# Kernel optimization log

Hardware: AMD Instinct MI355X
Metric: run time of the kernel (lower is better)

## Reference

```python
import jax, jax.numpy as jnp
import numpy as np

N = 100000   # nodes
E = 1600000  # edges (avg degree 16)
F = 128      # num_node_features
H = 128      # hid_size
G = 512      # num graphs in batch
C = 10       # num_classes
D = 32       # graph_degree_distribution.shape[1]
BN_EPS = 1e-5


def setup_inputs() -> dict:
    key = jax.random.key(0)
    ks = jax.random.split(key, 16)
    p = lambda k, shp: jax.random.normal(k, shp, jnp.float32) * 0.02
    x = jax.random.normal(ks[0], (N, F), jnp.float32)
    edge_index = jax.random.randint(ks[1], (2, E), 0, N)
    batch = jnp.sort(jax.random.randint(ks[2], (N,), 0, G))
    degree = jax.random.uniform(ks[3], (N,), jnp.float32) * 10.0
    return dict(
        x=x, edge_index=edge_index, batch=batch, degree=degree,
        eps1=jnp.zeros(()), W1a=p(ks[4], (F, H)), b1a=jnp.zeros(H), W1b=p(ks[5], (H, H)), b1b=jnp.zeros(H),
        g1=jnp.ones(H), be1=jnp.zeros(H),
        eps2=jnp.zeros(()), W2a=p(ks[6], (H, H)), b2a=jnp.zeros(H), W2b=p(ks[7], (H, H)), b2b=jnp.zeros(H),
        g2=jnp.ones(H), be2=jnp.zeros(H),
        Wlin1=p(ks[8], (H, H)), blin1=jnp.zeros(H),
        Wlin2=p(ks[9], (H, C)), blin2=jnp.zeros(C),
        Wlin4=p(ks[10], (H, D)), blin4=jnp.zeros(D),
        Wloss=p(ks[11], (H, 1)), bloss=jnp.zeros(1),
    )


def gin_conv(x, src, dst, eps, Wa, ba, Wb, bb, gamma, beta):
    # GINConv: MLP((1+eps)*x_i + sum_{j->i} x_j); MLP = Lin-ReLU-Lin-ReLU-BN
    agg = jax.ops.segment_sum(x[src], dst, num_segments=x.shape[0])  # [N,F] gather-scatter
    h = (1.0 + eps) * x + agg
    h = jax.nn.relu(h @ Wa + ba)
    h = jax.nn.relu(h @ Wb + bb)
    mu = h.mean(0)
    var = h.var(0)  # biased var, training-mode BN
    return gamma * (h - mu) * jax.lax.rsqrt(var + BN_EPS) + beta


def reference(x, edge_index, batch, degree,
              eps1, W1a, b1a, W1b, b1b, g1, be1,
              eps2, W2a, b2a, W2b, b2b, g2, be2,
              Wlin1, blin1, Wlin2, blin2, Wlin4, blin4, Wloss, bloss):
    src, dst = edge_index[0], edge_index[1]
    h = gin_conv(x, src, dst, eps1, W1a, b1a, W1b, b1b, g1, be1)
    h = gin_conv(h, src, dst, eps2, W2a, b2a, W2b, b2b, g2, be2)
    mse_x = h @ Wloss + bloss                       # [N,1]
    mse_loss = jnp.mean((mse_x - degree[:, None]) ** 2)
    # global_mean_pool over graphs
    sums = jax.ops.segment_sum(h, batch, num_segments=G)
    cnts = jax.ops.segment_sum(jnp.ones((h.shape[0], 1), h.dtype), batch, num_segments=G)
    g = sums / jnp.maximum(cnts, 1.0)               # [G,H]
    z = jax.nn.relu(g @ Wlin1 + blin1)              # dropout inert (eval)
    result1 = jax.nn.log_softmax(z @ Wlin2 + blin2, axis=-1)  # [G,C]
    result3 = z @ Wlin4 + blin4                      # [G,D]
    return result1, result3, mse_loss
```

## Files before the change

kernel.cpp:

```cpp
#include <hip/hip_runtime.h>
#include <hip/hip_bf16.h>

#define HF 128
#define BSH 8
#define BSZ 256
#define NBMAX 1024
#define FCAP 8192
#define AST 136
#define HB 512

typedef __attribute__((ext_vector_type(8))) short bf16x8;
typedef __attribute__((ext_vector_type(4))) float f32x4;
typedef __attribute__((ext_vector_type(2))) float f32x2;

__device__ inline float bflo(unsigned u) { return __uint_as_float(u << 16); }
__device__ inline float bfhi(unsigned u) { return __uint_as_float(u & 0xffff0000u); }
__device__ inline unsigned short f2bf(float f) {
    unsigned u = __float_as_uint(f);
    unsigned r = (u + 0x7fffu + ((u >> 16) & 1u)) >> 16;
    return (unsigned short)r;
}
__device__ inline unsigned pack2(float a, float b) {
    return (unsigned)f2bf(a) | ((unsigned)f2bf(b) << 16);
}
__device__ inline uint2 pk8_fp8(const float* v) {
    int a = __builtin_amdgcn_cvt_pk_fp8_f32(v[0], v[1], 0, 0);
    a = __builtin_amdgcn_cvt_pk_fp8_f32(v[2], v[3], a, 1);
    int b = __builtin_amdgcn_cvt_pk_fp8_f32(v[4], v[5], 0, 0);
    b = __builtin_amdgcn_cvt_pk_fp8_f32(v[6], v[7], b, 1);
    uint2 r; r.x = (unsigned)a; r.y = (unsigned)b;
    return r;
}

__global__ __launch_bounds__(256) void init_all(
    const float* __restrict__ x, unsigned short* __restrict__ xb,
    unsigned char* __restrict__ x8, int castBlk, int nchunks,
    const float* __restrict__ w0, const float* __restrict__ w1,
    const float* __restrict__ w2, const float* __restrict__ w3,
    unsigned short* __restrict__ WtAll,
    const int* __restrict__ dst, int* __restrict__ bpart, int E, int chunkH,
    const int* __restrict__ batch, int* __restrict__ gstart, int N, int Gn, int nBlocks,
    float* __restrict__ Szero, float* __restrict__ outm)
{
    __shared__ int lh[NBMAX];
    int b = blockIdx.x;
    int t = threadIdx.x;
    if (b < castBlk) {
        int i = b * 256 + t;
        if (i < nchunks) {
            float4 a = ((const float4*)x)[2 * i];
            float4 c = ((const float4*)x)[2 * i + 1];
            uint4 o;
            o.x = pack2(a.x, a.y); o.y = pack2(a.z, a.w);
            o.z = pack2(c.x, c.y); o.w = pack2(c.z, c.w);
            ((uint4*)xb)[i] = o;
            float v[8] = {a.x, a.y, a.z, a.w, c.x, c.y, c.z, c.w};
            ((uint2*)x8)[i] = pk8_fp8(v);
        }
        return;
    }
    b -= castBlk;
    if (b < 4) {
        const float* W = (b == 0) ? w0 : (b == 1) ? w1 : (b == 2) ? w2 : w3;
        unsigned short* O = WtAll + b * 16384;
        for (int idx = t; idx < 16384; idx += 256) {
            int n = idx >> 7, k = idx & 127;
            O[idx] = f2bf(W[k * 128 + n]);
        }
        return;
    }
    b -= 4;
    if (b < HB) {
        int NBl = (N + BSZ - 1) >> BSH;
        for (int i = t; i < NBl; i += 256) lh[i] = 0;
        __syncthreads();
        int beg = b * chunkH;
        int end = min(E, beg + chunkH);
        for (int e = beg + t; e < end; e += 256)
            atomicAdd(&lh[dst[e] >> BSH], 1);
        __syncthreads();
        for (int i = t; i < NBl; i += 256) bpart[i * HB + b] = lh[i];
        return;
    }
    b -= HB;
    if (b < nBlocks) {
        int i = b * 256 + t;
        if (i >= N) return;
        int bi = batch[i];
        int bp = (i == 0) ? -1 : batch[i - 1];
        for (int g = bp + 1; g <= bi; g++) gstart[g] = i;
        if (i == N - 1)
            for (int g = bi + 1; g <= Gn; g++) gstart[g] = N;
        return;
    }
    if (t < 2 * HF) { Szero[t] = 0.f; Szero[t + 2 * HF] = 0.f; }
    if (t == 0) outm[0] = 0.f;
}

__global__ void scanp(const int* __restrict__ bpart, int* __restrict__ boff,
                      int* __restrict__ bcur, int NB, int E)
{
    __shared__ int tot[NBMAX];
    __shared__ int part[256];
    int t = threadIdx.x;
    for (int i = t; i < NB; i += 256) {
        const int4* pp = (const int4*)(bpart + (size_t)i * HB);
        int run = 0;
#pragma unroll 4
        for (int b = 0; b < HB / 4; b++) {
            int4 v = pp[b];
            run += v.x + v.y + v.z + v.w;
        }
        tot[i] = run;
    }
    __syncthreads();
    int v[4];
    int s = 0;
#pragma unroll
    for (int i = 0; i < 4; i++) {
        int idx = t * 4 + i;
        v[i] = (idx < NB) ? tot[idx] : 0;
        s += v[i];
    }
    part[t] = s;
    __syncthreads();
    for (int o = 1; o < 256; o <<= 1) {
        int y = (t >= o) ? part[t - o] : 0;
        __syncthreads();
        part[t] += y;
        __syncthreads();
    }
    int base = part[t] - s;
#pragma unroll
    for (int i = 0; i < 4; i++) {
        int idx = t * 4 + i;
        if (idx < NB) { boff[idx] = base; bcur[idx] = base; base += v[i]; }
    }
    if (t == 0) boff[NB] = E;
}

__global__ __launch_bounds__(256) void bucket_bin(
    const int* __restrict__ src, const int* __restrict__ dst,
    int* __restrict__ bcur, unsigned* __restrict__ ebuf, int E, int NB, int chunkH)
{
    __shared__ int lh[NBMAX];
    int t = threadIdx.x;
    for (int i = t; i < NB; i += 256) lh[i] = 0;
    __syncthreads();
    int beg = blockIdx.x * chunkH;
    int end = min(E, beg + chunkH);
    for (int e = beg + t; e < end; e += 256)
        atomicAdd(&lh[dst[e] >> BSH], 1);
    __syncthreads();
    for (int i = t; i < NB; i += 256) {
        int c = lh[i];
        lh[i] = c ? atomicAdd(&bcur[i], c) : 0;
    }
    __syncthreads();
    for (int e = beg + t; e < end; e += 256) {
        int d = dst[e];
        int b = d >> BSH;
        int pos = atomicAdd(&lh[b], 1);
        ebuf[pos] = ((unsigned)src[e] << BSH) | (unsigned)(d & (BSZ - 1));
    }
}

__global__ __launch_bounds__(256) void bucket_fill(
    const unsigned* __restrict__ ebuf, const int* __restrict__ boff,
    int* __restrict__ off, int* __restrict__ esrc, int N, int NB, int E)
{
    __shared__ int deg[BSZ];
    __shared__ int pref[BSZ];
    __shared__ int lcur[BSZ];
    __shared__ int lsr[FCAP];
    int b = blockIdx.x;
    int t = threadIdx.x;
    int segBeg = boff[b], segEnd = boff[b + 1];
    int segLen = segEnd - segBeg;
    int node0 = b << BSH;
    deg[t] = 0;
    __syncthreads();
    for (int i = segBeg + t; i < segEnd; i += 256)
        atomicAdd(&deg[ebuf[i] & (BSZ - 1)], 1);
    __syncthreads();
    int dv = deg[t];
    pref[t] = dv;
    __syncthreads();
    for (int o = 1; o < 256; o <<= 1) {
        int y = (t >= o) ? pref[t - o] : 0;
        __syncthreads();
        pref[t] += y;
        __syncthreads();
    }
    int excl = pref[t] - dv;
    int node = node0 + t;
    if (node < N) off[node] = segBeg + excl;
    lcur[t] = excl;
    if (b == NB - 1 && t == 0) off[N] = E;
    __syncthreads();
    if (segLen <= FCAP) {
        for (int i = segBeg + t; i < segEnd; i += 256) {
            unsigned v = ebuf[i];
            int slot = atomicAdd(&lcur[v & (BSZ - 1)], 1);
            lsr[slot] = (int)(v >> BSH);
        }
        __syncthreads();
        for (int i = t; i < segLen; i += 256) esrc[segBeg + i] = lsr[i];
    } else {
        for (int i = segBeg + t; i < segEnd; i += 256) {
            unsigned v = ebuf[i];
            int slot = atomicAdd(&lcur[v & (BSZ - 1)], 1);
            esrc[segBeg + slot] = (int)(v >> BSH);
        }
    }
}

template <bool FOLD>
__global__ __launch_bounds__(256) void gather_u(
    const unsigned short* __restrict__ xb, const unsigned char* __restrict__ x8,
    const int* __restrict__ off, const int* __restrict__ esrc,
    const float* __restrict__ epsp,
    const float* __restrict__ S1, const float* __restrict__ S2,
    const float* __restrict__ gamma, const float* __restrict__ beta, float invN,
    unsigned short* __restrict__ Uo, int N)
{
    __shared__ float lsc[HF], lsh[HF];
    int tid = threadIdx.x;
    if (FOLD) {
        if (tid < HF) {
            float mu = S1[tid] * invN;
            float var = S2[tid] * invN - mu * mu;
            float rs = rsqrtf(var + 1e-5f);
            float sc = gamma[tid] * rs;
            lsc[tid] = sc;
            lsh[tid] = beta[tid] - mu * sc;
        }
        __syncthreads();
    }
    int lane16 = tid & 15;
    int node = (blockIdx.x * 256 + tid) >> 4;
    if (node >= N) return;
    int beg = off[node], end = off[node + 1];
    float acc[8] = {0.f, 0.f, 0.f, 0.f, 0.f, 0.f, 0.f, 0.f};
    for (int j0 = beg; j0 < end; j0 += 16) {
        int myidx = (j0 + lane16 < end) ? esrc[j0 + lane16] : 0;
        int cnt = min(16, end - j0);
        for (int t = 0; t < cnt; t++) {
            int s = __shfl(myidx, t, 16);
            uint2 p = *(const uint2*)(x8 + (size_t)s * HF + lane16 * 8);
            f32x2 f0 = __builtin_amdgcn_cvt_pk_f32_fp8((int)p.x, 0);
            f32x2 f1 = __builtin_amdgcn_cvt_pk_f32_fp8((int)p.x, 1);
            f32x2 f2 = __builtin_amdgcn_cvt_pk_f32_fp8((int)p.y, 0);
            f32x2 f3 = __builtin_amdgcn_cvt_pk_f32_fp8((int)p.y, 1);
            acc[0] += f0.x; acc[1] += f0.y;
            acc[2] += f1.x; acc[3] += f1.y;
            acc[4] += f2.x; acc[5] += f2.y;
            acc[6] += f3.x; acc[7] += f3.y;
        }
    }
    float ep = 1.0f + epsp[0];
    uint4 xx = *(const uint4*)(xb + (size_t)node * HF + lane16 * 8);
    acc[0] += ep * bflo(xx.x); acc[1] += ep * bfhi(xx.x);
    acc[2] += ep * bflo(xx.y); acc[3] += ep * bfhi(xx.y);
    acc[4] += ep * bflo(xx.z); acc[5] += ep * bfhi(xx.z);
    acc[6] += ep * bflo(xx.w); acc[7] += ep * bfhi(xx.w);
    if (FOLD) {
        float cf = ep + (float)(end - beg);
        const float4 s0 = *(const float4*)(&lsc[lane16 * 8]);
        const float4 s1 = *(const float4*)(&lsc[lane16 * 8 + 4]);
        const float4 h0 = *(const float4*)(&lsh[lane16 * 8]);
        const float4 h1 = *(const float4*)(&lsh[lane16 * 8 + 4]);
        acc[0] = acc[0] * s0.x + h0.x * cf; acc[1] = acc[1] * s0.y + h0.y * cf;
        acc[2] = acc[2] * s0.z + h0.z * cf; acc[3] = acc[3] * s0.w + h0.w * cf;
        acc[4] = acc[4] * s1.x + h1.x * cf; acc[5] = acc[5] * s1.y + h1.y * cf;
        acc[6] = acc[6] * s1.z + h1.z * cf; acc[7] = acc[7] * s1.w + h1.w * cf;
    }
    uint4 o;
    o.x = pack2(acc[0], acc[1]); o.y = pack2(acc[2], acc[3]);
    o.z = pack2(acc[4], acc[5]); o.w = pack2(acc[6], acc[7]);
    *(uint4*)(Uo + (size_t)node * HF + lane16 * 8) = o;
}

__global__ __launch_bounds__(256) void gemm2L(
    const unsigned short* __restrict__ U,
    const unsigned short* __restrict__ Wta, const float* __restrict__ ba,
    const unsigned short* __restrict__ Wtb, const float* __restrict__ bb,
    unsigned short* __restrict__ out, unsigned char* __restrict__ out8,
    float* __restrict__ S1, float* __restrict__ S2, int n)
{
    __shared__ unsigned short lW[128 * AST];
    __shared__ unsigned short lT[64 * AST];
    __shared__ float lS1[HF], lS2[HF];
    int tid = threadIdx.x;
    int w = tid >> 6, lane = tid & 63;
    int m = lane & 15, quad = lane >> 4;
    int row0 = blockIdx.x * 64;
    if (tid < HF) { lS1[tid] = 0.f; lS2[tid] = 0.f; }

    for (int c = tid; c < 2048; c += 256) {
        int r = c >> 4, k16 = c & 15;
        *(uint4*)(&lW[r * AST + k16 * 8]) = *(const uint4*)(Wta + r * HF + k16 * 8);
    }
    __syncthreads();

    int arow = row0 + w * 16 + m;
    if (arow >= n) arow = n - 1;
    bf16x8 aF[4];
#pragma unroll
    for (int kk = 0; kk < 4; kk++)
        aF[kk] = *(const bf16x8*)(U + (size_t)arow * HF + kk * 32 + quad * 8);

    f32x4 acc[8];
#pragma unroll
    for (int nt = 0; nt < 8; nt++) acc[nt] = (f32x4){0.f, 0.f, 0.f, 0.f};
#pragma unroll
    for (int nt = 0; nt < 8; nt++) {
#pragma unroll
        for (int kk = 0; kk < 4; kk++) {
            bf16x8 b = *(const bf16x8*)(&lW[(nt * 16 + m) * AST + kk * 32 + quad * 8]);
            acc[nt] = __builtin_amdgcn_mfma_f32_16x16x32_bf16(aF[kk], b, acc[nt], 0, 0, 0);
        }
    }
#pragma unroll
    for (int nt = 0; nt < 8; nt++) {
        float bav = ba[nt * 16 + m];
#pragma unroll
        for (int r = 0; r < 4; r++) {
            int lrow = w * 16 + quad * 4 + r;
            lT[lrow * AST + nt * 16 + m] = f2bf(fmaxf(acc[nt][r] + bav, 0.f));
        }
    }
    __syncthreads();
    for (int c = tid; c < 2048; c += 256) {
        int r = c >> 4, k16 = c & 15;
        *(uint4*)(&lW[r * AST + k16 * 8]) = *(const uint4*)(Wtb + r * HF + k16 * 8);
    }
    __syncthreads();

#pragma unroll
    for (int kk = 0; kk < 4; kk++)
        aF[kk] = *(const bf16x8*)(&lT[(w * 16 + m) * AST + kk * 32 + quad * 8]);
#pragma unroll
    for (int nt = 0; nt < 8; nt++) acc[nt] = (f32x4){0.f, 0.f, 0.f, 0.f};
#pragma unroll
    for (int nt = 0; nt < 8; nt++) {
#pragma unroll
        for (int kk = 0; kk < 4; kk++) {
            bf16x8 b = *(const bf16x8*)(&lW[(nt * 16 + m) * AST + kk * 32 + quad * 8]);
            acc[nt] = __builtin_amdgcn_mfma_f32_16x16x32_bf16(aF[kk], b, acc[nt], 0, 0, 0);
        }
    }
#pragma unroll
    for (int nt = 0; nt < 8; nt++) {
        int col = nt * 16 + m;
        float bbv = bb[col];
        float cs = 0.f, cq = 0.f;
#pragma unroll
        for (int r = 0; r < 4; r++) {
            int lrow = w * 16 + quad * 4 + r;
            int grow = row0 + lrow;
            float v = fmaxf(acc[nt][r] + bbv, 0.f);
            lT[lrow * AST + col] = f2bf(v);
            if (grow < n) { cs += v; cq += v * v; }
        }
        cs += __shfl_down(cs, 32); cs += __shfl_down(cs, 16);
        cq += __shfl_down(cq, 32); cq += __shfl_down(cq, 16);
        if (quad == 0) { atomicAdd(&lS1[col], cs); atomicAdd(&lS2[col], cq); }
    }
#pragma unroll
    for (int i = 0; i < 4; i++) {
        int idx = i * 64 + lane;
        int r = idx >> 4, k16 = idx & 15;
        int grow = row0 + w * 16 + r;
        if (grow < n) {
            uint4 v = *(const uint4*)(&lT[(w * 16 + r) * AST + k16 * 8]);
            *(uint4*)(out + (size_t)grow * HF + k16 * 8) = v;
            if (out8) {
                float f[8] = {bflo(v.x), bfhi(v.x), bflo(v.y), bfhi(v.y),
                              bflo(v.z), bfhi(v.z), bflo(v.w), bfhi(v.w)};
                *(uint2*)(out8 + (size_t)grow * HF + k16 * 8) = pk8_fp8(f);
            }
        }
    }
    __syncthreads();
    if (tid < HF) { atomicAdd(&S1[tid], lS1[tid]); atomicAdd(&S2[tid], lS2[tid]); }
}

__global__ __launch_bounds__(512) void pool_tail(
    const unsigned short* __restrict__ h2raw,
    const float* __restrict__ S1, const float* __restrict__ S2,
    const float* __restrict__ gamma, const float* __restrict__ beta, float invN,
    const int* __restrict__ gstart, const float* __restrict__ W,
    const float* __restrict__ bias,
    const float* __restrict__ Wloss, const float* __restrict__ blossp,
    const float* __restrict__ degree,
    const float* __restrict__ W2, const float* __restrict__ b2,
    const float* __restrict__ W4, const float* __restrict__ b4,
    float* __restrict__ out1, float* __restrict__ out3,
    float* __restrict__ outm, int C_, int D_)
{
    __shared__ float lsc[HF], lsh[HF];
    __shared__ float red[8][HF];
    __shared__ float gv[HF];
    __shared__ float part[4][HF];
    __shared__ float wred[8];
    __shared__ float zz[HF];
    __shared__ float logits[16];
    __shared__ float lse_s;
    int gid = blockIdx.x;
    int t = threadIdx.x;
    if (t < HF) {
        float mu = S1[t] * invN;
        float var = S2[t] * invN - mu * mu;
        float rs = rsqrtf(var + 1e-5f);
        float sc = gamma[t] * rs;
        lsc[t] = sc;
        lsh[t] = beta[t] - mu * sc;
    }
    __syncthreads();
    int c2 = t & 63;
    int rg = t >> 6;
    int b = gstart[gid], e = gstart[gid + 1];
    float wla = lsc[2 * c2] * Wloss[2 * c2];
    float wlb = lsc[2 * c2 + 1] * Wloss[2 * c2 + 1];
    float c0l = lsh[2 * c2] * Wloss[2 * c2] + lsh[2 * c2 + 1] * Wloss[2 * c2 + 1];
    float bl = blossp[0];
    float s0 = 0.f, s1 = 0.f, macc = 0.f;
    for (int r = b + rg; r < e; r += 8) {
        unsigned u = *(const unsigned*)(h2raw + (size_t)r * HF + c2 * 2);
        float v0 = bflo(u), v1 = bfhi(u);
        s0 += v0; s1 += v1;
        float m = v0 * wla + v1 * wlb + c0l;
#pragma unroll
        for (int o = 32; o > 0; o >>= 1) m += __shfl_down(m, o);
        if (c2 == 0) {
            float d = m + bl - degree[r];
            macc += d * d;
        }
    }
    red[rg][c2 * 2] = s0;
    red[rg][c2 * 2 + 1] = s1;
    if (c2 == 0) wred[rg] = macc;
    __syncthreads();
    if (t < HF) {
        float s = red[0][t] + red[1][t] + red[2][t] + red[3][t]
                + red[4][t] + red[5][t] + red[6][t] + red[7][t];
        gv[t] = (e > b) ? lsc[t] * (s / (float)(e - b)) + lsh[t] : 0.f;
    }
    __syncthreads();
    int c = t & 127, kg = t >> 7;
    float a = 0.f;
#pragma unroll 8
    for (int k = kg * 32; k < kg * 32 + 32; k++) a += gv[k] * W[(size_t)k * HF + c];
    part[kg][c] = a;
    __syncthreads();
    if (t < HF) {
        float aa = part[0][t] + part[1][t] + part[2][t] + part[3][t] + bias[t];
        zz[t] = fmaxf(aa, 0.f);
    }
    if (t == 0) {
        float ps = wred[0] + wred[1] + wred[2] + wred[3]
                 + wred[4] + wred[5] + wred[6] + wred[7];
        atomicAdd(outm, ps * invN);
    }
    __syncthreads();
    if (t < C_) {
        float aa = b2[t];
        for (int k = 0; k < HF; k++) aa += zz[k] * W2[(size_t)k * C_ + t];
        logits[t] = aa;
    }
    __syncthreads();
    if (t == 0) {
        float mx = -1e30f;
        for (int i = 0; i < C_; i++) mx = fmaxf(mx, logits[i]);
        float s = 0.f;
        for (int i = 0; i < C_; i++) s += expf(logits[i] - mx);
        lse_s = mx + logf(s);
    }
    __syncthreads();
    if (t < C_) out1[(size_t)gid * C_ + t] = logits[t] - lse_s;
    if (t < D_) {
        float aa = b4[t];
        for (int k = 0; k < HF; k++) aa += zz[k] * W4[(size_t)k * D_ + t];
        out3[(size_t)gid * D_ + t] = aa;
    }
}

extern "C" void kernel_launch(void* const* d_in, const int* in_sizes, int n_in,
                              void* d_out, int out_size, void* d_ws, size_t ws_size,
                              hipStream_t stream)
{
    const float* x      = (const float*)d_in[0];
    const int*   ei     = (const int*)d_in[1];
    const int*   batch  = (const int*)d_in[2];
    const float* degree = (const float*)d_in[3];
    const float* eps1   = (const float*)d_in[4];
    const float* W1a    = (const float*)d_in[5];
    const float* b1a    = (const float*)d_in[6];
    const float* W1b    = (const float*)d_in[7];
    const float* b1b    = (const float*)d_in[8];
    const float* g1     = (const float*)d_in[9];
    const float* be1    = (const float*)d_in[10];
    const float* eps2   = (const float*)d_in[11];
    const float* W2a    = (const float*)d_in[12];
    const float* b2a    = (const float*)d_in[13];
    const float* W2b    = (const float*)d_in[14];
    const float* b2b    = (const float*)d_in[15];
    const float* g2     = (const float*)d_in[16];
    const float* be2    = (const float*)d_in[17];
    const float* Wlin1  = (const float*)d_in[18];
    const float* blin1  = (const float*)d_in[19];
    const float* Wlin2  = (const float*)d_in[20];
    const float* blin2  = (const float*)d_in[21];
    const float* Wlin4  = (const float*)d_in[22];
    const float* blin4  = (const float*)d_in[23];
    const float* Wloss  = (const float*)d_in[24];
    const float* bloss  = (const float*)d_in[25];

    const int N  = in_sizes[0] / HF;
    const int E  = in_sizes[1] / 2;
    const int C_ = in_sizes[21];
    const int D_ = in_sizes[23];
    const int Gn = (out_size - 1) / (C_ + D_);
    const int NB = (N + BSZ - 1) >> BSH;

    const int* src = ei;
    const int* dst = ei + E;

    size_t NH = (size_t)N * HF;
    char* p = (char*)d_ws;
    unsigned short* xb  = (unsigned short*)p; p += NH * 2;
    unsigned short* U   = (unsigned short*)p; p += NH * 2;
    unsigned short* Hp1 = (unsigned short*)p; p += NH * 2;
    unsigned short* Hp2 = (unsigned short*)p; p += NH * 2;
    unsigned char*  x8  = (unsigned char*)p; p += NH;
    unsigned char*  h8  = (unsigned char*)p; p += NH;
    unsigned short* WtAll = (unsigned short*)p; p += 4 * 16384 * 2;
    float* S1a  = (float*)p; p += HF * 4;
    float* S2a  = (float*)p; p += HF * 4;
    float* S1b  = (float*)p; p += HF * 4;
    float* S2b  = (float*)p; p += HF * 4;
    int* gstart = (int*)p; p += (Gn + 1) * 4;
    int* boff   = (int*)p; p += (NBMAX + 1) * 4;
    int* bcur   = (int*)p; p += NBMAX * 4;
    int* bpart  = (int*)p; p += (size_t)NBMAX * HB * 4;
    int* off    = (int*)p; p += (N + 1) * 4;
    int* esrc   = (int*)p; p += E * 4;
    unsigned* ebuf = (unsigned*)p; p += E * 4;

    unsigned short* Wt1a = WtAll;
    unsigned short* Wt1b = WtAll + 16384;
    unsigned short* Wt2a = WtAll + 32768;
    unsigned short* Wt2b = WtAll + 49152;

    float* out1 = (float*)d_out;
    float* out3 = out1 + (size_t)Gn * C_;
    float* outm = out3 + (size_t)Gn * D_;

    int nchunks  = (int)(NH / 8);
    int castBlk  = (nchunks + 255) / 256;
    int nBlocks  = (N + 255) / 256;
    int gatherBlk = (N * 16 + 255) / 256;
    int gemmBlk  = (N + 63) / 64;
    int chunkH   = (E + HB - 1) / HB;
    float invN = 1.0f / (float)N;

    int initBlk = castBlk + 4 + HB + nBlocks + 1;

    init_all<<<initBlk, 256, 0, stream>>>(x, xb, x8, castBlk, nchunks,
                                          W1a, W1b, W2a, W2b, WtAll,
                                          dst, bpart, E, chunkH,
                                          batch, gstart, N, Gn, nBlocks,
                                          S1a, outm);
    scanp<<<1, 256, 0, stream>>>(bpart, boff, bcur, NB, E);
    bucket_bin<<<HB, 256, 0, stream>>>(src, dst, bcur, ebuf, E, NB, chunkH);
    bucket_fill<<<NB, 256, 0, stream>>>(ebuf, boff, off, esrc, N, NB, E);
    gather_u<false><<<gatherBlk, 256, 0, stream>>>(xb, x8, off, esrc, eps1,
                                                   nullptr, nullptr, nullptr, nullptr, 0.f, U, N);
    gemm2L<<<gemmBlk, 256, 0, stream>>>(U, Wt1a, b1a, Wt1b, b1b, Hp1, h8, S1a, S2a, N);
    gather_u<true><<<gatherBlk, 256, 0, stream>>>(Hp1, h8, off, esrc, eps2,
                                                  S1a, S2a, g1, be1, invN, U, N);
    gemm2L<<<gemmBlk, 256, 0, stream>>>(U, Wt2a, b2a, Wt2b, b2b, Hp2, nullptr, S1b, S2b, N);
    pool_tail<<<Gn, 512, 0, stream>>>(Hp2, S1b, S2b, g2, be2, invN, gstart,
                                      Wlin1, blin1, Wloss, bloss, degree,
                                      Wlin2, blin2, Wlin4, blin4,
                                      out1, out3, outm, C_, D_);
}
```

Baseline: 473.2 us.

## Make fused MLP GEMM persistent with pre-swizzled fragment weights and per-wave tiles

The fused two-layer MLP kernel becomes persistent: 512 blocks keep both weight matrices resident in LDS, and each wave loops over 16-row tiles while prefetching the next tile's A fragments. The weight pre-transform now writes weights in MFMA fragment order, so B loads are contiguous per lane. The intermediate tile moves to a per-wave XOR-swizzled LDS buffer, which removes the block-level syncs and weight reloads. BatchNorm statistics are held in registers and flushed with global atomics once per wave. The costs are higher LDS use per block (about 80 KB), which limits occupancy, and tail imbalance from the fixed grid.

```diff
diff --git a/kernel.cpp b/kernel.cpp
--- a/kernel.cpp
+++ b/kernel.cpp
@@ -6,7 +6,6 @@
 #define BSZ 256
 #define NBMAX 1024
 #define FCAP 8192
-#define AST 136
 #define HB 512
 
 typedef __attribute__((ext_vector_type(8))) short bf16x8;
@@ -64,8 +63,14 @@
         const float* W = (b == 0) ? w0 : (b == 1) ? w1 : (b == 2) ? w2 : w3;
         unsigned short* O = WtAll + b * 16384;
         for (int idx = t; idx < 16384; idx += 256) {
-            int n = idx >> 7, k = idx & 127;
-            O[idx] = f2bf(W[k * 128 + n]);
+            int j    = idx & 7;
+            int lane = (idx >> 3) & 63;
+            int fk   = idx >> 9;
+            int kk = fk & 3, nt = fk >> 2;
+            int m = lane & 15, quad = lane >> 4;
+            int ncol = nt * 16 + m;
+            int krow = kk * 32 + quad * 8 + j;
+            O[idx] = f2bf(W[krow * 128 + ncol]);
         }
         return;
     }
@@ -283,107 +288,134 @@
 
 __global__ __launch_bounds__(256) void gemm2L(
     const unsigned short* __restrict__ U,
-    const unsigned short* __restrict__ Wta, const float* __restrict__ ba,
-    const unsigned short* __restrict__ Wtb, const float* __restrict__ bb,
+    const unsigned short* __restrict__ Wfa, const float* __restrict__ ba,
+    const unsigned short* __restrict__ Wfb, const float* __restrict__ bb,
     unsigned short* __restrict__ out, unsigned char* __restrict__ out8,
     float* __restrict__ S1, float* __restrict__ S2, int n)
 {
-    __shared__ unsigned short lW[128 * AST];
-    __shared__ unsigned short lT[64 * AST];
-    __shared__ float lS1[HF], lS2[HF];
+    __shared__ __align__(16) unsigned short lWa[16384];
+    __shared__ __align__(16) unsigned short lWb[16384];
+    __shared__ __align__(16) unsigned short lT[8192];
     int tid = threadIdx.x;
     int w = tid >> 6, lane = tid & 63;
     int m = lane & 15, quad = lane >> 4;
-    int row0 = blockIdx.x * 64;
-    if (tid < HF) { lS1[tid] = 0.f; lS2[tid] = 0.f; }
-
-    for (int c = tid; c < 2048; c += 256) {
-        int r = c >> 4, k16 = c & 15;
-        *(uint4*)(&lW[r * AST + k16 * 8]) = *(const uint4*)(Wta + r * HF + k16 * 8);
-    }
-    __syncthreads();
-
-    int arow = row0 + w * 16 + m;
-    if (arow >= n) arow = n - 1;
+
+    for (int i = tid; i < 2048; i += 256) {
+        ((uint4*)lWa)[i] = ((const uint4*)Wfa)[i];
+        ((uint4*)lWb)[i] = ((const uint4*)Wfb)[i];
+    }
+    __syncthreads();
+
+    float bav[8], bbv[8];
+#pragma unroll
+    for (int nt = 0; nt < 8; nt++) { bav[nt] = ba[nt * 16 + m]; bbv[nt] = bb[nt * 16 + m]; }
+
+    unsigned short* lTw = lT + w * 2048;
+    int swzA = (m & 7) << 3;
+
+    float csA[8], cqA[8];
+#pragma unroll
+    for (int nt = 0; nt < 8; nt++) { csA[nt] = 0.f; cqA[nt] = 0.f; }
+
+    int wid = (blockIdx.x << 2) | w;
+    int nw = gridDim.x << 2;
+    int ntiles = (n + 15) >> 4;
+
     bf16x8 aF[4];
-#pragma unroll
-    for (int kk = 0; kk < 4; kk++)
-        aF[kk] = *(const bf16x8*)(U + (size_t)arow * HF + kk * 32 + quad * 8);
-
-    f32x4 acc[8];
-#pragma unroll
-    for (int nt = 0; nt < 8; nt++) acc[nt] = (f32x4){0.f, 0.f, 0.f, 0.f};
-#pragma unroll
-    for (int nt = 0; nt < 8; nt++) {
-#pragma unroll
-        for (int kk = 0; kk < 4; kk++) {
-            bf16x8 b = *(const bf16x8*)(&lW[(nt * 16 + m) * AST + kk * 32 + quad * 8]);
-            acc[nt] = __builtin_amdgcn_mfma_f32_16x16x32_bf16(aF[kk], b, acc[nt], 0, 0, 0);
-        }
-    }
-#pragma unroll
-    for (int nt = 0; nt < 8; nt++) {
-        float bav = ba[nt * 16 + m];
-#pragma unroll
-        for (int r = 0; r < 4; r++) {
-            int lrow = w * 16 + quad * 4 + r;
-            lT[lrow * AST + nt * 16 + m] = f2bf(fmaxf(acc[nt][r] + bav, 0.f));
-        }
-    }
-    __syncthreads();
-    for (int c = tid; c < 2048; c += 256) {
-        int r = c >> 4, k16 = c & 15;
-        *(uint4*)(&lW[r * AST + k16 * 8]) = *(const uint4*)(Wtb + r * HF + k16 * 8);
-    }
-    __syncthreads();
-
-#pragma unroll
-    for (int kk = 0; kk < 4; kk++)
-        aF[kk] = *(const bf16x8*)(&lT[(w * 16 + m) * AST + kk * 32 + quad * 8]);
-#pragma unroll
-    for (int nt = 0; nt < 8; nt++) acc[nt] = (f32x4){0.f, 0.f, 0.f, 0.f};
-#pragma unroll
-    for (int nt = 0; nt < 8; nt++) {
-#pragma unroll
-        for (int kk = 0; kk < 4; kk++) {
-            bf16x8 b = *(const bf16x8*)(&lW[(nt * 16 + m) * AST + kk * 32 + quad * 8]);
-            acc[nt] = __builtin_amdgcn_mfma_f32_16x16x32_bf16(aF[kk], b, acc[nt], 0, 0, 0);
-        }
-    }
-#pragma unroll
-    for (int nt = 0; nt < 8; nt++) {
-        int col = nt * 16 + m;
-        float bbv = bb[col];
-        float cs = 0.f, cq = 0.f;
-#pragma unroll
-        for (int r = 0; r < 4; r++) {
-            int lrow = w * 16 + quad * 4 + r;
-            int grow = row0 + lrow;
-            float v = fmaxf(acc[nt][r] + bbv, 0.f);
-            lT[lrow * AST + col] = f2bf(v);
-            if (grow < n) { cs += v; cq += v * v; }
-        }
-        cs += __shfl_down(cs, 32); cs += __shfl_down(cs, 16);
-        cq += __shfl_down(cq, 32); cq += __shfl_down(cq, 16);
-        if (quad == 0) { atomicAdd(&lS1[col], cs); atomicAdd(&lS2[col], cq); }
-    }
-#pragma unroll
-    for (int i = 0; i < 4; i++) {
-        int idx = i * 64 + lane;
-        int r = idx >> 4, k16 = idx & 15;
-        int grow = row0 + w * 16 + r;
-        if (grow < n) {
-            uint4 v = *(const uint4*)(&lT[(w * 16 + r) * AST + k16 * 8]);
-            *(uint4*)(out + (size_t)grow * HF + k16 * 8) = v;
-            if (out8) {
-                float f[8] = {bflo(v.x), bfhi(v.x), bflo(v.y), bfhi(v.y),
-                              bflo(v.z), bfhi(v.z), bflo(v.w), bfhi(v.w)};
-                *(uint2*)(out8 + (size_t)grow * HF + k16 * 8) = pk8_fp8(f);
+    int tile = wid;
+    if (tile < ntiles) {
+        int ar = tile * 16 + m; if (ar >= n) ar = n - 1;
+        const unsigned short* up = U + (size_t)ar * HF + quad * 8;
+#pragma unroll
+        for (int kk = 0; kk < 4; kk++) aF[kk] = *(const bf16x8*)(up + kk * 32);
+    }
+
+    for (; tile < ntiles; tile += nw) {
+        bf16x8 aN[4];
+        {
+            int tn = tile + nw;
+            int tl = (tn < ntiles) ? tn : tile;
+            int ar = tl * 16 + m; if (ar >= n) ar = n - 1;
+            const unsigned short* up = U + (size_t)ar * HF + quad * 8;
+#pragma unroll
+            for (int kk = 0; kk < 4; kk++) aN[kk] = *(const bf16x8*)(up + kk * 32);
+        }
+
+        f32x4 acc[8];
+#pragma unroll
+        for (int nt = 0; nt < 8; nt++) acc[nt] = (f32x4){0.f, 0.f, 0.f, 0.f};
+#pragma unroll
+        for (int nt = 0; nt < 8; nt++) {
+#pragma unroll
+            for (int kk = 0; kk < 4; kk++) {
+                bf16x8 b = *(const bf16x8*)(&lWa[((((nt << 2) | kk) << 6) | lane) << 3]);
+                acc[nt] = __builtin_amdgcn_mfma_f32_16x16x32_bf16(aF[kk], b, acc[nt], 0, 0, 0);
             }
         }
-    }
-    __syncthreads();
-    if (tid < HF) { atomicAdd(&S1[tid], lS1[tid]); atomicAdd(&S2[tid], lS2[tid]); }
+#pragma unroll
+        for (int nt = 0; nt < 8; nt++) {
+#pragma unroll
+            for (int r = 0; r < 4; r++) {
+                int row = (quad << 2) | r;
+                lTw[(row << 7) | ((nt * 16 + m) ^ ((row & 7) << 3))] =
+                    f2bf(fmaxf(acc[nt][r] + bav[nt], 0.f));
+            }
+        }
+        bf16x8 a2[4];
+#pragma unroll
+        for (int kk = 0; kk < 4; kk++)
+            a2[kk] = *(const bf16x8*)(&lTw[(m << 7) | (((kk << 5) | (quad << 3)) ^ swzA)]);
+#pragma unroll
+        for (int nt = 0; nt < 8; nt++) acc[nt] = (f32x4){0.f, 0.f, 0.f, 0.f};
+#pragma unroll
+        for (int nt = 0; nt < 8; nt++) {
+#pragma unroll
+            for (int kk = 0; kk < 4; kk++) {
+                bf16x8 b = *(const bf16x8*)(&lWb[((((nt << 2) | kk) << 6) | lane) << 3]);
+                acc[nt] = __builtin_amdgcn_mfma_f32_16x16x32_bf16(a2[kk], b, acc[nt], 0, 0, 0);
+            }
+        }
+        int row0 = tile << 4;
+#pragma unroll
+        for (int nt = 0; nt < 8; nt++) {
+            float cs = 0.f, cq = 0.f;
+#pragma unroll
+            for (int r = 0; r < 4; r++) {
+                int row = (quad << 2) | r;
+                float v = fmaxf(acc[nt][r] + bbv[nt], 0.f);
+                lTw[(row << 7) | ((nt * 16 + m) ^ ((row & 7) << 3))] = f2bf(v);
+                if (row0 + row < n) { cs += v; cq += v * v; }
+            }
+            cs += __shfl_down(cs, 32); cs += __shfl_down(cs, 16);
+            cq += __shfl_down(cq, 32); cq += __shfl_down(cq, 16);
+            csA[nt] += cs; cqA[nt] += cq;
+        }
+#pragma unroll
+        for (int i = 0; i < 4; i++) {
+            int chunk = (i << 6) | lane;
+            int row = chunk >> 4, c16 = chunk & 15;
+            int grow = row0 + row;
+            if (grow < n) {
+                uint4 v = *(const uint4*)(&lTw[(row << 7) | (((c16 << 3) ^ ((row & 7) << 3)))]);
+                *(uint4*)(out + (size_t)grow * HF + (c16 << 3)) = v;
+                if (out8) {
+                    float f[8] = {bflo(v.x), bfhi(v.x), bflo(v.y), bfhi(v.y),
+                                  bflo(v.z), bfhi(v.z), bflo(v.w), bfhi(v.w)};
+                    *(uint2*)(out8 + (size_t)grow * HF + (c16 << 3)) = pk8_fp8(f);
+                }
+            }
+        }
+#pragma unroll
+        for (int kk = 0; kk < 4; kk++) aF[kk] = aN[kk];
+    }
+
+    if (quad == 0) {
+#pragma unroll
+        for (int nt = 0; nt < 8; nt++) {
+            atomicAdd(&S1[nt * 16 + m], csA[nt]);
+            atomicAdd(&S2[nt * 16 + m], cqA[nt]);
+        }
+    }
 }
 
 __global__ __launch_bounds__(512) void pool_tail(
@@ -561,7 +593,7 @@
     int castBlk  = (nchunks + 255) / 256;
     int nBlocks  = (N + 255) / 256;
     int gatherBlk = (N * 16 + 255) / 256;
-    int gemmBlk  = (N + 63) / 64;
+    int gemmBlk  = 512;
     int chunkH   = (E + HB - 1) / HB;
     float invN = 1.0f / (float)N;
 
```

Result: slower. 492.0 us (+4.0%).
